# Kernel tuning notes

Measured on AMD Instinct MI355X. Metric: run time of the kernel, lower is better.

## Reference

```python
import jax, jax.numpy as jnp
import numpy as np

B, L, DIM = 2, 2048, 2048
H, KV, HD = 32, 8, 64
N_REP = H // KV


def setup_inputs() -> dict:
    key = jax.random.key(0)
    ks = jax.random.split(key, 6)
    std = DIM ** -0.5
    std_o = (H * HD) ** -0.5 / np.sqrt(2 * 24)
    x = jax.random.normal(ks[0], (B, L, DIM), dtype=jnp.float32)
    # freqs_cis packs (cos, sin), each [L, head_dim//2]
    pos = jnp.arange(L, dtype=jnp.float32)[:, None]
    inv = 1.0 / (10000.0 ** (jnp.arange(0, HD, 2, dtype=jnp.float32) / HD))
    ang = pos * inv[None, :]
    freqs_cis = jnp.stack([jnp.cos(ang), jnp.sin(ang)], axis=0)
    wq = jax.random.normal(ks[1], (H * HD, DIM), dtype=jnp.float32) * std
    wk = jax.random.normal(ks[2], (KV * HD, DIM), dtype=jnp.float32) * std
    wv = jax.random.normal(ks[3], (KV * HD, DIM), dtype=jnp.float32) * std
    wo = jax.random.normal(ks[4], (DIM, H * HD), dtype=jnp.float32) * std_o
    return {"x": x, "freqs_cis": freqs_cis, "wq": wq, "wk": wk, "wv": wv, "wo": wo}


def _rope(t, cos, sin):
    # t: [B, L, h, HD]; interleaved (real, imag) pairs in last dim
    tr = t.reshape(*t.shape[:-1], HD // 2, 2)
    out_r = tr[..., 0] * cos - tr[..., 1] * sin
    out_i = tr[..., 0] * sin + tr[..., 1] * cos
    return jnp.stack([out_r, out_i], axis=-1).reshape(t.shape)


def reference(x, freqs_cis, wq, wk, wv, wo):
    Bb, Ll, _ = x.shape
    xq = (x @ wq.T).reshape(Bb, Ll, H, HD)
    xk = (x @ wk.T).reshape(Bb, Ll, KV, HD)
    xv = (x @ wv.T).reshape(Bb, Ll, KV, HD)
    cos = freqs_cis[0].reshape(1, Ll, 1, HD // 2)
    sin = freqs_cis[1].reshape(1, Ll, 1, HD // 2)
    xq = _rope(xq, cos, sin)
    xk = _rope(xk, cos, sin)
    # GQA: repeat_interleave kv heads to n_heads
    xk = jnp.repeat(xk, N_REP, axis=2)
    xv = jnp.repeat(xv, N_REP, axis=2)
    scale = 1.0 / jnp.sqrt(jnp.asarray(HD, x.dtype))
    scores = jnp.einsum('bihd,bjhd->bhij', xq, xk) * scale
    causal = jnp.tril(jnp.ones((Ll, Ll), dtype=bool))
    scores = jnp.where(causal[None, None], scores, jnp.finfo(scores.dtype).min)
    attn = jax.nn.softmax(scores, axis=-1)
    out = jnp.einsum('bhij,bjhd->bihd', attn, xv).reshape(Bb, Ll, H * HD)
    return out @ wo.T
```

## Files before the change

### kernel.cpp

```cpp
#include <hip/hip_runtime.h>
#include <stdint.h>

typedef __bf16 bf16;
typedef __attribute__((ext_vector_type(8))) __bf16 bf16x8;
typedef __attribute__((ext_vector_type(4))) __bf16 bf16x4;
typedef __attribute__((ext_vector_type(4))) short short4v;
typedef __attribute__((ext_vector_type(4))) float f32x4;

static constexpr int Bn = 2, Ln = 2048, DIMn = 2048, Hn = 32, KVn = 8, HDn = 64;
static constexpr int TS = 3072;

#if defined(__has_builtin)
#if __has_builtin(__builtin_amdgcn_exp2f)
#define EXP2(x) __builtin_amdgcn_exp2f(x)
#endif
#endif
#ifndef EXP2
#define EXP2(x) exp2f(x)
#endif

#define TO_LDS(p) ((__attribute__((address_space(3))) uint32_t*)(uintptr_t)(p))
#define TO_GLB(p) ((const __attribute__((address_space(1))) uint32_t*)(uintptr_t)(p))

__global__ void cast_all(const float* __restrict__ x, const float* __restrict__ wq,
                         const float* __restrict__ wk, const float* __restrict__ wv,
                         const float* __restrict__ wo, bf16* __restrict__ xb,
                         bf16* __restrict__ wqkvb, bf16* __restrict__ wob) {
    size_t i = (size_t)(blockIdx.x * blockDim.x + threadIdx.x) * 4;
    const float* src;
    bf16* dst;
    if (i < 8388608) {
        src = x + i; dst = xb + i;
    } else if (i < 8388608 + 6291456) {
        size_t j = i - 8388608;
        dst = wqkvb + j;
        if (j < 4194304)      src = wq + j;
        else if (j < 5242880) src = wk + (j - 4194304);
        else                  src = wv + (j - 5242880);
    } else {
        size_t j = i - 14680064;
        src = wo + j; dst = wob + j;
    }
    float4 v = *(const float4*)src;
    bf16 o[4] = {(bf16)v.x, (bf16)v.y, (bf16)v.z, (bf16)v.w};
    *(uint64_t*)dst = *(uint64_t*)o;
}

__global__ void rope_k(bf16* __restrict__ qkv, const float* __restrict__ fc) {
    int idx = blockIdx.x * blockDim.x + threadIdx.x;
    int i   = idx & 31;
    int kvh = (idx >> 5) & 7;
    int bl  = idx >> 8;
    int l   = bl & (Ln - 1);
    size_t base = (size_t)bl * TS + 2048 + kvh * 64 + 2 * i;
    float cr = fc[l * 32 + i];
    float sr = fc[65536 + l * 32 + i];
    float x0 = (float)qkv[base], x1 = (float)qkv[base + 1];
    qkv[base]     = (bf16)(x0 * cr - x1 * sr);
    qkv[base + 1] = (bf16)(x0 * sr + x1 * cr);
}

template <bool OUT_BF16>
__global__ __launch_bounds__(256) void gemm_bt(const bf16* __restrict__ A,
                                               const bf16* __restrict__ Bm,
                                               void* __restrict__ C,
                                               int M, int N, int K) {
    __shared__ bf16 sA[128 * 32];
    __shared__ bf16 sB[128 * 32];
    const int t    = threadIdx.x;
    const int wave = t >> 6, lane = t & 63;
    const int q4 = lane >> 4, l16 = lane & 15;
    const int bm = blockIdx.y * 128, bn = blockIdx.x * 128;
    const int wm = (wave >> 1) * 64, wn = (wave & 1) * 64;

    f32x4 acc[4][4] = {};

    const int srow = wave * 16 + (lane >> 2);
    const int scol = (lane & 3) * 8;
    const bf16* pa = A + (size_t)(bm + srow) * K + scol;
    const bf16* pb = Bm + (size_t)(bn + srow) * K + scol;
    bf16* la = &sA[wave * 16 * 32];
    bf16* lb = &sB[wave * 16 * 32];

    for (int k0 = 0; k0 < K; k0 += 32) {
#pragma unroll
        for (int p = 0; p < 2; ++p) {
            __builtin_amdgcn_global_load_lds(TO_GLB(pa + (size_t)p * 64 * K),
                                             TO_LDS(la + p * 64 * 32), 16, 0, 0);
            __builtin_amdgcn_global_load_lds(TO_GLB(pb + (size_t)p * 64 * K),
                                             TO_LDS(lb + p * 64 * 32), 16, 0, 0);
        }
        pa += 32; pb += 32;
        __syncthreads();
        bf16x8 af[4], bfr[4];
#pragma unroll
        for (int i = 0; i < 4; ++i) {
            af[i]  = *(const bf16x8*)(&sA[(wm + i * 16 + l16) * 32 + q4 * 8]);
            bfr[i] = *(const bf16x8*)(&sB[(wn + i * 16 + l16) * 32 + q4 * 8]);
        }
#pragma unroll
        for (int mi = 0; mi < 4; ++mi)
#pragma unroll
            for (int ni = 0; ni < 4; ++ni)
                acc[mi][ni] = __builtin_amdgcn_mfma_f32_16x16x32_bf16(af[mi], bfr[ni],
                                                                      acc[mi][ni], 0, 0, 0);
        __syncthreads();
    }

#pragma unroll
    for (int mi = 0; mi < 4; ++mi)
#pragma unroll
        for (int ni = 0; ni < 4; ++ni)
#pragma unroll
            for (int r = 0; r < 4; ++r) {
                size_t row = bm + wm + mi * 16 + q4 * 4 + r;
                size_t col = bn + wn + ni * 16 + l16;
                if (OUT_BF16)
                    ((bf16*)C)[row * N + col] = (bf16)acc[mi][ni][r];
                else
                    ((float*)C)[row * N + col] = acc[mi][ni][r];
            }
}

__global__ __launch_bounds__(256, 2) void attn_kernel(const bf16* __restrict__ QKV,
                                                      const float* __restrict__ fc,
                                                      bf16* __restrict__ O) {
    constexpr int LDK = 72;
    __shared__ bf16 sK[64 * LDK];
    __shared__ bf16 sV[64 * LDK];
    const int t    = threadIdx.x;
    const int wave = t >> 6, lane = t & 63;
    const int q4 = lane >> 4, l16 = lane & 15;
    const int hidx = wave & 1, qh = wave >> 1;
    const int L = blockIdx.x;
    const int pair = L & 15, hp = (L >> 4) & 1, kvh = (L >> 5) & 7, b = L >> 8;
    const int h = kvh * 4 + hp * 2 + hidx;
    constexpr float SC = 0.125f * 1.44269504088896340736f;

    const bf16* kb = QKV + (size_t)(b * Ln) * TS + 2048 + kvh * 64;
    const bf16* vb = kb + 512;
    const int krow = t >> 3;
    const int kc8  = (t & 7) * 8;
    const int vkey = t & 63, vhd0 = (t >> 6) * 16;

    for (int half = 0; half < 2; ++half) {
        const int qtile = half == 0 ? 31 - pair : pair;

        bf16x8 qf[2][2];
#pragma unroll
        for (int g2 = 0; g2 < 2; ++g2) {
            int ql = qtile * 64 + (qh * 2 + g2) * 16 + l16;
            const bf16* qp = QKV + (size_t)(b * Ln + ql) * TS + h * 64;
#pragma unroll
            for (int hc = 0; hc < 2; ++hc) {
                bf16x8 raw = *(const bf16x8*)(qp + hc * 32 + q4 * 8);
                float4 c4 = *(const float4*)(fc + ql * 32 + hc * 16 + q4 * 4);
                float4 s4 = *(const float4*)(fc + 65536 + ql * 32 + hc * 16 + q4 * 4);
                bf16x8 o;
#pragma unroll
                for (int m = 0; m < 4; ++m) {
                    float cr = ((const float*)&c4)[m], sr = ((const float*)&s4)[m];
                    float x0 = (float)raw[2 * m], x1 = (float)raw[2 * m + 1];
                    o[2 * m]     = (bf16)((x0 * cr - x1 * sr) * SC);
                    o[2 * m + 1] = (bf16)((x0 * sr + x1 * cr) * SC);
                }
                qf[g2][hc] = o;
            }
        }

        f32x4 o_acc[2][4] = {};
        float l_r[2] = {0.f, 0.f};

        bf16x8 kreg[2], vreg[2];
#pragma unroll
        for (int p = 0; p < 2; ++p)
            kreg[p] = *(const bf16x8*)(kb + (size_t)(p * 32 + krow) * TS + kc8);
        {
            const bf16* v0 = vb + (size_t)vkey * TS + vhd0;
            vreg[0] = *(const bf16x8*)(v0);
            vreg[1] = *(const bf16x8*)(v0 + 8);
        }

        for (int kt = 0; kt <= qtile; ++kt) {
#pragma unroll
            for (int p = 0; p < 2; ++p)
                *(float4*)(&sK[(p * 32 + krow) * LDK + kc8]) = *(float4*)&kreg[p];
            {
                bf16 vv[16];
                *(bf16x8*)(vv)     = vreg[0];
                *(bf16x8*)(vv + 8) = vreg[1];
#pragma unroll
                for (int j = 0; j < 16; ++j) sV[(vhd0 + j) * LDK + vkey] = vv[j];
            }
            __syncthreads();

            if (kt < qtile) {
#pragma unroll
                for (int p = 0; p < 2; ++p)
                    kreg[p] = *(const bf16x8*)(kb + (size_t)((kt + 1) * 64 + p * 32 + krow) * TS + kc8);
                const bf16* v0 = vb + (size_t)((kt + 1) * 64 + vkey) * TS + vhd0;
                vreg[0] = *(const bf16x8*)(v0);
                vreg[1] = *(const bf16x8*)(v0 + 8);
            }

            bf16x8 kf[4][2];
#pragma unroll
            for (int c = 0; c < 4; ++c)
#pragma unroll
                for (int hc = 0; hc < 2; ++hc)
                    kf[c][hc] = *(const bf16x8*)(&sK[(c * 16 + l16) * LDK + hc * 32 + q4 * 8]);
            short4v vf[4][4];
#pragma unroll
            for (int nc = 0; nc < 4; ++nc)
#pragma unroll
                for (int c = 0; c < 4; ++c)
                    vf[nc][c] = *(const short4v*)(&sV[(nc * 16 + l16) * LDK + c * 16 + q4 * 4]);

            const bool diag = (kt == qtile);
#pragma unroll
            for (int g2 = 0; g2 < 2; ++g2) {
                f32x4 s[4];
#pragma unroll
                for (int c = 0; c < 4; ++c) {
                    f32x4 a = {};
                    a = __builtin_amdgcn_mfma_f32_16x16x32_bf16(kf[c][0], qf[g2][0], a, 0, 0, 0);
                    a = __builtin_amdgcn_mfma_f32_16x16x32_bf16(kf[c][1], qf[g2][1], a, 0, 0, 0);
                    s[c] = a;
                }
                int qrow = qtile * 64 + (qh * 2 + g2) * 16 + l16;
                float lsum = 0.f;
                short4v pb4[4];
#pragma unroll
                for (int c = 0; c < 4; ++c)
#pragma unroll
                    for (int r = 0; r < 4; ++r) {
                        float p = EXP2(s[c][r] - 12.f);
                        if (diag && (kt * 64 + c * 16 + q4 * 4 + r > qrow)) p = 0.f;
                        lsum += p;
                        bf16 ph = (bf16)p;
                        pb4[c][r] = *(const short*)&ph;
                    }
                l_r[g2] += lsum;
#pragma unroll
                for (int nc = 0; nc < 4; ++nc)
#pragma unroll
                    for (int c = 0; c < 4; ++c)
                        o_acc[g2][nc] = __builtin_amdgcn_mfma_f32_16x16x16bf16_1k(
                            vf[nc][c], pb4[c], o_acc[g2][nc], 0, 0, 0);
            }
            __syncthreads();
        }

#pragma unroll
        for (int g2 = 0; g2 < 2; ++g2) {
            float l = l_r[g2];
            l += __shfl_xor(l, 16, 64);
            l += __shfl_xor(l, 32, 64);
            float inv = 1.f / l;
            int qrow = qtile * 64 + (qh * 2 + g2) * 16 + l16;
            bf16* op = O + (size_t)(b * Ln + qrow) * (Hn * HDn) + h * 64;
#pragma unroll
            for (int nc = 0; nc < 4; ++nc) {
                bf16x4 o;
#pragma unroll
                for (int r = 0; r < 4; ++r) o[r] = (bf16)(o_acc[g2][nc][r] * inv);
                *(bf16x4*)(op + nc * 16 + q4 * 4) = o;
            }
        }
    }
}

extern "C" void kernel_launch(void* const* d_in, const int* in_sizes, int n_in,
                              void* d_out, int out_size, void* d_ws, size_t ws_size,
                              hipStream_t stream) {
    const float* x  = (const float*)d_in[0];
    const float* fc = (const float*)d_in[1];
    const float* wq = (const float*)d_in[2];
    const float* wk = (const float*)d_in[3];
    const float* wv = (const float*)d_in[4];
    const float* wo = (const float*)d_in[5];
    float* out = (float*)d_out;

    const size_t T = (size_t)Bn * Ln;
    char* p = (char*)d_ws;
    bf16* xb    = (bf16*)p; p += T * DIMn * 2;
    bf16* wqkvb = (bf16*)p; p += (size_t)TS * DIMn * 2;
    bf16* wob   = (bf16*)p; p += (size_t)DIMn * Hn * HDn * 2;
    bf16* qkv   = (bf16*)p; p += T * TS * 2;
    bf16* ao    = (bf16*)p; p += T * Hn * HDn * 2;

    cast_all<<<dim3(18432), dim3(256), 0, stream>>>(x, wq, wk, wv, wo, xb, wqkvb, wob);

    gemm_bt<true><<<dim3(TS / 128, 32), dim3(256), 0, stream>>>(xb, wqkvb, qkv, 4096, TS, 2048);

    rope_k<<<dim3(4096), dim3(256), 0, stream>>>(qkv, fc);

    attn_kernel<<<dim3(512), dim3(256), 0, stream>>>(qkv, fc, ao);

    gemm_bt<false><<<dim3(16, 32), dim3(256), 0, stream>>>(ao, wob, out, 4096, 2048, 2048);
}
```

Measured before the change: 304.3 us.

## Replace GEMM with 256x256-tile double-buffered, swizzled, prioritized MFMA kernel

Both projection GEMMs now use a 512-thread kernel with 256x256 output tiles and a K step of 64. The A and B tiles are double-buffered in LDS through async global-to-LDS loads, with an XOR swizzle to avoid bank conflicts. The MFMA work is split into four quadrants separated by barriers with s_setprio, and the next-tile loads are interleaved between them to overlap memory with compute. The bigger tiles raise data reuse per block, but they cut the grid to 192 and 128 blocks and use about 128KB of LDS, which may leave many CUs idle.

```diff
diff --git a/kernel.cpp b/kernel.cpp
--- a/kernel.cpp
+++ b/kernel.cpp
@@ -60,65 +60,144 @@
     qkv[base + 1] = (bf16)(x0 * sr + x1 * cr);
 }
 
+static __device__ __forceinline__ void barrier_f() {
+    asm volatile("" ::: "memory");
+    __builtin_amdgcn_s_barrier();
+    asm volatile("" ::: "memory");
+}
+
 template <bool OUT_BF16>
-__global__ __launch_bounds__(256) void gemm_bt(const bf16* __restrict__ A,
-                                               const bf16* __restrict__ Bm,
-                                               void* __restrict__ C,
-                                               int M, int N, int K) {
-    __shared__ bf16 sA[128 * 32];
-    __shared__ bf16 sB[128 * 32];
+__global__ __launch_bounds__(512, 2) void gemm256(const bf16* __restrict__ A,
+                                                  const bf16* __restrict__ Bm,
+                                                  void* __restrict__ C,
+                                                  int M, int N, int K) {
+    (void)M;
+    __shared__ bf16 sA[2][256 * 64];
+    __shared__ bf16 sB[2][256 * 64];
     const int t    = threadIdx.x;
     const int wave = t >> 6, lane = t & 63;
     const int q4 = lane >> 4, l16 = lane & 15;
-    const int bm = blockIdx.y * 128, bn = blockIdx.x * 128;
-    const int wm = (wave >> 1) * 64, wn = (wave & 1) * 64;
-
-    f32x4 acc[4][4] = {};
-
-    const int srow = wave * 16 + (lane >> 2);
-    const int scol = (lane & 3) * 8;
-    const bf16* pa = A + (size_t)(bm + srow) * K + scol;
-    const bf16* pb = Bm + (size_t)(bn + srow) * K + scol;
-    bf16* la = &sA[wave * 16 * 32];
-    bf16* lb = &sB[wave * 16 * 32];
-
-    for (int k0 = 0; k0 < K; k0 += 32) {
-#pragma unroll
-        for (int p = 0; p < 2; ++p) {
-            __builtin_amdgcn_global_load_lds(TO_GLB(pa + (size_t)p * 64 * K),
-                                             TO_LDS(la + p * 64 * 32), 16, 0, 0);
-            __builtin_amdgcn_global_load_lds(TO_GLB(pb + (size_t)p * 64 * K),
-                                             TO_LDS(lb + p * 64 * 32), 16, 0, 0);
-        }
-        pa += 32; pb += 32;
-        __syncthreads();
-        bf16x8 af[4], bfr[4];
-#pragma unroll
-        for (int i = 0; i < 4; ++i) {
-            af[i]  = *(const bf16x8*)(&sA[(wm + i * 16 + l16) * 32 + q4 * 8]);
-            bfr[i] = *(const bf16x8*)(&sB[(wn + i * 16 + l16) * 32 + q4 * 8]);
-        }
+    const int wm = wave >> 2, wn = wave & 3;
+    const int r8  = lane >> 3;
+    const int csw = ((lane & 7) ^ r8) * 8;
+
+    const size_t bm = (size_t)blockIdx.y * 256, bn = (size_t)blockIdx.x * 256;
+    const bf16* pa = A  + (bm + (size_t)(wave * 16 + r8)) * K + csw;
+    const bf16* pb = Bm + (bn + (size_t)(wave * 16 + r8)) * K + csw;
+    const int NT = K >> 6;
+
+#define STG(P, SX, cbuf, h, i, kt)                                                            \
+    __builtin_amdgcn_global_load_lds(                                                          \
+        TO_GLB(P + (size_t)((h) * 128 + (i) * 8) * K + (size_t)(kt) * 64),                     \
+        TO_LDS(&SX[cbuf][((h) * 128 + wave * 16 + (i) * 8) * 64]), 16, 0, 0)
+
+#pragma unroll
+    for (int kt = 0; kt < 2; ++kt)
+#pragma unroll
+        for (int h = 0; h < 2; ++h)
+#pragma unroll
+            for (int i = 0; i < 2; ++i) {
+                STG(pa, sA, kt, h, i, kt);
+                STG(pb, sB, kt, h, i, kt);
+            }
+    asm volatile("s_waitcnt vmcnt(8)" ::: "memory");
+    __builtin_amdgcn_s_barrier();
+    asm volatile("" ::: "memory");
+
+    f32x4 acc[8][4] = {};
+    bf16x8 af[8][2], bfr[4][2];
+
+#define MMQ(m0, n0)                                                                            \
+    _Pragma("unroll") for (int mi = 0; mi < 4; ++mi)                                           \
+    _Pragma("unroll") for (int ni = 0; ni < 2; ++ni)                                           \
+    _Pragma("unroll") for (int kk = 0; kk < 2; ++kk)                                           \
+        acc[(m0) + mi][(n0) + ni] = __builtin_amdgcn_mfma_f32_16x16x32_bf16(                   \
+            af[(m0) + mi][kk], bfr[(n0) + ni][kk], acc[(m0) + mi][(n0) + ni], 0, 0, 0)
+
+    for (int k = 0; k < NT; ++k) {
+        const int c = k & 1;
+        const bf16* la = &sA[c][0];
+        const bf16* lb = &sB[c][0];
+        const int swz = (l16 & 7);
+
 #pragma unroll
         for (int mi = 0; mi < 4; ++mi)
 #pragma unroll
-            for (int ni = 0; ni < 4; ++ni)
-                acc[mi][ni] = __builtin_amdgcn_mfma_f32_16x16x32_bf16(af[mi], bfr[ni],
-                                                                      acc[mi][ni], 0, 0, 0);
-        __syncthreads();
+            for (int kk = 0; kk < 2; ++kk)
+                af[mi][kk] = *(const bf16x8*)(la + (wm * 128 + mi * 16 + l16) * 64 +
+                                              ((kk * 4 + q4) ^ swz) * 8);
+#pragma unroll
+        for (int ni = 0; ni < 2; ++ni)
+#pragma unroll
+            for (int kk = 0; kk < 2; ++kk)
+                bfr[ni][kk] = *(const bf16x8*)(lb + (wn * 64 + ni * 16 + l16) * 64 +
+                                               ((kk * 4 + q4) ^ swz) * 8);
+        barrier_f();
+        __builtin_amdgcn_s_setprio(1);
+        MMQ(0, 0);
+        __builtin_amdgcn_s_setprio(0);
+        barrier_f();
+
+#pragma unroll
+        for (int mi = 0; mi < 4; ++mi)
+#pragma unroll
+            for (int kk = 0; kk < 2; ++kk)
+                af[4 + mi][kk] = *(const bf16x8*)(la + (wm * 128 + (4 + mi) * 16 + l16) * 64 +
+                                                  ((kk * 4 + q4) ^ swz) * 8);
+#pragma unroll
+        for (int ni = 0; ni < 2; ++ni)
+#pragma unroll
+            for (int kk = 0; kk < 2; ++kk)
+                bfr[2 + ni][kk] = *(const bf16x8*)(lb + (wn * 64 + (2 + ni) * 16 + l16) * 64 +
+                                                   ((kk * 4 + q4) ^ swz) * 8);
+        barrier_f();
+        __builtin_amdgcn_s_setprio(1);
+        MMQ(4, 2);
+        __builtin_amdgcn_s_setprio(0);
+        barrier_f();
+
+        if (k + 2 < NT) {
+            STG(pa, sA, c, 0, 0, k + 2);
+            STG(pa, sA, c, 0, 1, k + 2);
+            STG(pa, sA, c, 1, 0, k + 2);
+            STG(pa, sA, c, 1, 1, k + 2);
+        }
+        barrier_f();
+        __builtin_amdgcn_s_setprio(1);
+        MMQ(4, 0);
+        __builtin_amdgcn_s_setprio(0);
+        barrier_f();
+
+        if (k + 2 < NT) {
+            STG(pb, sB, c, 0, 0, k + 2);
+            STG(pb, sB, c, 0, 1, k + 2);
+            STG(pb, sB, c, 1, 0, k + 2);
+            STG(pb, sB, c, 1, 1, k + 2);
+            asm volatile("s_waitcnt vmcnt(8)" ::: "memory");
+        } else if (k == NT - 2) {
+            asm volatile("s_waitcnt vmcnt(0)" ::: "memory");
+        }
+        barrier_f();
+        __builtin_amdgcn_s_setprio(1);
+        MMQ(0, 2);
+        __builtin_amdgcn_s_setprio(0);
+        barrier_f();
     }
-
-#pragma unroll
-    for (int mi = 0; mi < 4; ++mi)
+#undef MMQ
+#undef STG
+
+#pragma unroll
+    for (int mi = 0; mi < 8; ++mi)
 #pragma unroll
         for (int ni = 0; ni < 4; ++ni)
 #pragma unroll
             for (int r = 0; r < 4; ++r) {
-                size_t row = bm + wm + mi * 16 + q4 * 4 + r;
-                size_t col = bn + wn + ni * 16 + l16;
+                size_t row = bm + wm * 128 + mi * 16 + q4 * 4 + r;
+                size_t col = bn + wn * 64 + ni * 16 + l16;
                 if (OUT_BF16)
-                    ((bf16*)C)[row * N + col] = (bf16)acc[mi][ni][r];
+                    ((bf16*)C)[row * (size_t)N + col] = (bf16)acc[mi][ni][r];
                 else
-                    ((float*)C)[row * N + col] = acc[mi][ni][r];
+                    ((float*)C)[row * (size_t)N + col] = acc[mi][ni][r];
             }
 }
 
@@ -291,11 +370,11 @@
 
     cast_all<<<dim3(18432), dim3(256), 0, stream>>>(x, wq, wk, wv, wo, xb, wqkvb, wob);
 
-    gemm_bt<true><<<dim3(TS / 128, 32), dim3(256), 0, stream>>>(xb, wqkvb, qkv, 4096, TS, 2048);
+    gemm256<true><<<dim3(TS / 256, 16), dim3(512), 0, stream>>>(xb, wqkvb, qkv, 4096, TS, 2048);
 
     rope_k<<<dim3(4096), dim3(256), 0, stream>>>(qkv, fc);
 
     attn_kernel<<<dim3(512), dim3(256), 0, stream>>>(qkv, fc, ao);
 
-    gemm_bt<false><<<dim3(16, 32), dim3(256), 0, stream>>>(ao, wob, out, 4096, 2048, 2048);
-}
+    gemm256<false><<<dim3(2048 / 256, 16), dim3(512), 0, stream>>>(ao, wob, out, 4096, 2048, 2048);
+}
```

New measurement: 302.9 us. About the same (-0.5%).

## Replace GEMM with double-buffered, swizzled 512-thread kernel with larger tiles

Applied to the files above, without the earlier changes.

Replaces the single-buffered 128x128 GEMM with a 512-thread kernel that uses larger tiles (256x192 for the QKV projection, 128x256 for the output projection) and a BK=64 K-step. Loads run double-buffered through global_load_lds with explicit vmcnt waits, so the next tile streams in while MFMAs run. An XOR swizzle on the LDS columns reduces bank conflicts. The larger register and LDS footprint may limit occupancy, and the grids shrink to 256 blocks each, which can leave part of the device idle.

```diff
diff --git a/kernel.cpp b/kernel.cpp
--- a/kernel.cpp
+++ b/kernel.cpp
@@ -60,65 +60,123 @@
     qkv[base + 1] = (bf16)(x0 * sr + x1 * cr);
 }
 
-template <bool OUT_BF16>
-__global__ __launch_bounds__(256) void gemm_bt(const bf16* __restrict__ A,
-                                               const bf16* __restrict__ Bm,
-                                               void* __restrict__ C,
-                                               int M, int N, int K) {
-    __shared__ bf16 sA[128 * 32];
-    __shared__ bf16 sB[128 * 32];
+static __device__ __forceinline__ void barrier_f() {
+    asm volatile("" ::: "memory");
+    __builtin_amdgcn_s_barrier();
+    asm volatile("" ::: "memory");
+}
+
+template <int N>
+static __device__ __forceinline__ void waitcnt_vm() {
+    if constexpr (N == 0) asm volatile("s_waitcnt vmcnt(0)" ::: "memory");
+    else if constexpr (N == 6) asm volatile("s_waitcnt vmcnt(6)" ::: "memory");
+    else if constexpr (N == 7) asm volatile("s_waitcnt vmcnt(7)" ::: "memory");
+    else static_assert(N == 0 || N == 6 || N == 7, "add vmcnt literal");
+}
+
+template <int BM, int BN, bool OUT_BF16>
+__global__ __launch_bounds__(512, 2) void gemm256(const bf16* __restrict__ A,
+                                                  const bf16* __restrict__ Bm,
+                                                  void* __restrict__ C,
+                                                  int M, int N, int K) {
+    (void)M;
+    constexpr int MI = BM / 32;
+    constexpr int NI = BN / 64;
+    constexpr int AJ = BM / 64, BJ = BN / 64, LPT = AJ + BJ;
+    __shared__ bf16 sA[2][BM * 64];
+    __shared__ bf16 sB[2][BN * 64];
     const int t    = threadIdx.x;
     const int wave = t >> 6, lane = t & 63;
     const int q4 = lane >> 4, l16 = lane & 15;
-    const int bm = blockIdx.y * 128, bn = blockIdx.x * 128;
-    const int wm = (wave >> 1) * 64, wn = (wave & 1) * 64;
-
-    f32x4 acc[4][4] = {};
-
-    const int srow = wave * 16 + (lane >> 2);
-    const int scol = (lane & 3) * 8;
-    const bf16* pa = A + (size_t)(bm + srow) * K + scol;
-    const bf16* pb = Bm + (size_t)(bn + srow) * K + scol;
-    bf16* la = &sA[wave * 16 * 32];
-    bf16* lb = &sB[wave * 16 * 32];
-
-    for (int k0 = 0; k0 < K; k0 += 32) {
-#pragma unroll
-        for (int p = 0; p < 2; ++p) {
-            __builtin_amdgcn_global_load_lds(TO_GLB(pa + (size_t)p * 64 * K),
-                                             TO_LDS(la + p * 64 * 32), 16, 0, 0);
-            __builtin_amdgcn_global_load_lds(TO_GLB(pb + (size_t)p * 64 * K),
-                                             TO_LDS(lb + p * 64 * 32), 16, 0, 0);
-        }
-        pa += 32; pb += 32;
-        __syncthreads();
-        bf16x8 af[4], bfr[4];
-#pragma unroll
-        for (int i = 0; i < 4; ++i) {
-            af[i]  = *(const bf16x8*)(&sA[(wm + i * 16 + l16) * 32 + q4 * 8]);
-            bfr[i] = *(const bf16x8*)(&sB[(wn + i * 16 + l16) * 32 + q4 * 8]);
-        }
-#pragma unroll
-        for (int mi = 0; mi < 4; ++mi)
-#pragma unroll
-            for (int ni = 0; ni < 4; ++ni)
-                acc[mi][ni] = __builtin_amdgcn_mfma_f32_16x16x32_bf16(af[mi], bfr[ni],
-                                                                      acc[mi][ni], 0, 0, 0);
-        __syncthreads();
+    const int wm = wave >> 2, wn = wave & 3;
+    const int r8l = lane >> 3;
+    const int csw = ((lane & 7) ^ r8l) * 8;
+
+    const size_t bm = (size_t)blockIdx.y * BM, bn = (size_t)blockIdx.x * BN;
+    const bf16* pa = A  + (bm + (size_t)(wave * 8 + r8l)) * K + csw;
+    const bf16* pb = Bm + (bn + (size_t)(wave * 8 + r8l)) * K + csw;
+    const int NT = K >> 6;
+
+#define STGA(buf, kt)                                                                          \
+    _Pragma("unroll") for (int j = 0; j < AJ; ++j)                                             \
+        __builtin_amdgcn_global_load_lds(TO_GLB(pa + (size_t)j * 64 * K + (size_t)(kt) * 64),  \
+                                         TO_LDS(&sA[buf][(j * 64 + wave * 8) * 64]), 16, 0, 0)
+#define STGB(buf, kt)                                                                          \
+    _Pragma("unroll") for (int j = 0; j < BJ; ++j)                                             \
+        __builtin_amdgcn_global_load_lds(TO_GLB(pb + (size_t)j * 64 * K + (size_t)(kt) * 64),  \
+                                         TO_LDS(&sB[buf][(j * 64 + wave * 8) * 64]), 16, 0, 0)
+
+    STGA(0, 0); STGB(0, 0);
+    STGA(1, 1); STGB(1, 1);
+    waitcnt_vm<LPT>();
+    __builtin_amdgcn_s_barrier();
+    asm volatile("" ::: "memory");
+
+    f32x4 acc[MI][NI] = {};
+    bf16x8 af[MI][2], bfr[NI][2];
+
+    for (int k = 0; k < NT; ++k) {
+        const int c = k & 1;
+        const bf16* la = &sA[c][0];
+        const bf16* lb = &sB[c][0];
+        const int sw = (l16 & 7);
+
+#pragma unroll
+        for (int mi = 0; mi < MI / 2; ++mi)
+#pragma unroll
+            for (int kk = 0; kk < 2; ++kk)
+                af[mi][kk] = *(const bf16x8*)(la + (wm * (BM / 2) + mi * 16 + l16) * 64 +
+                                              ((kk * 4 + q4) ^ sw) * 8);
+#pragma unroll
+        for (int ni = 0; ni < NI; ++ni)
+#pragma unroll
+            for (int kk = 0; kk < 2; ++kk)
+                bfr[ni][kk] = *(const bf16x8*)(lb + (wn * (BN / 4) + ni * 16 + l16) * 64 +
+                                               ((kk * 4 + q4) ^ sw) * 8);
+#pragma unroll
+        for (int mi = MI / 2; mi < MI; ++mi)
+#pragma unroll
+            for (int kk = 0; kk < 2; ++kk)
+                af[mi][kk] = *(const bf16x8*)(la + (wm * (BM / 2) + mi * 16 + l16) * 64 +
+                                              ((kk * 4 + q4) ^ sw) * 8);
+
+        __builtin_amdgcn_s_setprio(1);
+#pragma unroll
+        for (int mi = 0; mi < MI; ++mi)
+#pragma unroll
+            for (int ni = 0; ni < NI; ++ni)
+#pragma unroll
+                for (int kk = 0; kk < 2; ++kk)
+                    acc[mi][ni] = __builtin_amdgcn_mfma_f32_16x16x32_bf16(
+                        af[mi][kk], bfr[ni][kk], acc[mi][ni], 0, 0, 0);
+        __builtin_amdgcn_s_setprio(0);
+
+        barrier_f();
+
+        if (k + 2 < NT) {
+            STGA(c, k + 2);
+            STGB(c, k + 2);
+            waitcnt_vm<LPT>();
+        } else if (k == NT - 2) {
+            waitcnt_vm<0>();
+        }
+        barrier_f();
     }
-
-#pragma unroll
-    for (int mi = 0; mi < 4; ++mi)
-#pragma unroll
-        for (int ni = 0; ni < 4; ++ni)
+#undef STGA
+#undef STGB
+
+#pragma unroll
+    for (int mi = 0; mi < MI; ++mi)
+#pragma unroll
+        for (int ni = 0; ni < NI; ++ni)
 #pragma unroll
             for (int r = 0; r < 4; ++r) {
-                size_t row = bm + wm + mi * 16 + q4 * 4 + r;
-                size_t col = bn + wn + ni * 16 + l16;
+                size_t row = bm + wm * (BM / 2) + mi * 16 + q4 * 4 + r;
+                size_t col = bn + wn * (BN / 4) + ni * 16 + l16;
                 if (OUT_BF16)
-                    ((bf16*)C)[row * N + col] = (bf16)acc[mi][ni][r];
+                    ((bf16*)C)[row * (size_t)N + col] = (bf16)acc[mi][ni][r];
                 else
-                    ((float*)C)[row * N + col] = acc[mi][ni][r];
+                    ((float*)C)[row * (size_t)N + col] = acc[mi][ni][r];
             }
 }
 
@@ -291,11 +349,13 @@
 
     cast_all<<<dim3(18432), dim3(256), 0, stream>>>(x, wq, wk, wv, wo, xb, wqkvb, wob);
 
-    gemm_bt<true><<<dim3(TS / 128, 32), dim3(256), 0, stream>>>(xb, wqkvb, qkv, 4096, TS, 2048);
+    gemm256<256, 192, true><<<dim3(TS / 192, 4096 / 256), dim3(512), 0, stream>>>(
+        xb, wqkvb, qkv, 4096, TS, 2048);
 
     rope_k<<<dim3(4096), dim3(256), 0, stream>>>(qkv, fc);
 
     attn_kernel<<<dim3(512), dim3(256), 0, stream>>>(qkv, fc, ao);
 
-    gemm_bt<false><<<dim3(16, 32), dim3(256), 0, stream>>>(ao, wob, out, 4096, 2048, 2048);
-}
+    gemm256<128, 256, false><<<dim3(2048 / 256, 4096 / 128), dim3(512), 0, stream>>>(
+        ao, wob, out, 4096, 2048, 2048);
+}
```

Result: faster. 270.3 us (-11.2%).
